# Optimization experiments

Hardware: AMD Instinct MI355X
Metric: run time of the kernel (lower is better)

Reference implementation:

```python
import jax, jax.numpy as jnp
import numpy as np

N = 100000
E = 1600000
IN_CH = 128
HID = 128
HEADS = 4
C = HID // HEADS  # 32 per-head channels
NUM_CLASSES = 40
NEG_SLOPE = 0.2


def _glorot(key, shape):
    fan_in, fan_out = shape[0], shape[-1]
    lim = jnp.sqrt(6.0 / (fan_in + fan_out))
    return jax.random.uniform(key, shape, jnp.float32, -lim, lim)


def setup_inputs() -> dict:
    key = jax.random.key(0)
    ks = jax.random.split(key, 12)
    x = jax.random.normal(ks[0], (N, IN_CH), jnp.float32)
    edge_index = jax.random.randint(ks[1], (2, E), 0, N, jnp.int64)
    edge_weight = jax.random.uniform(ks[2], (E,), jnp.float32)
    return {
        'x': x,
        'edge_index': edge_index,
        'edge_weight': edge_weight,
        'W_pre': _glorot(ks[3], (IN_CH, HID)),
        'Wl': _glorot(ks[4], (HID, HEADS * C)),
        'bl': jnp.zeros((HEADS * C,), jnp.float32),
        'Wr': _glorot(ks[5], (HID, HEADS * C)),
        'br': jnp.zeros((HEADS * C,), jnp.float32),
        'We': _glorot(ks[6], (1, HEADS * C)),
        'att': _glorot(ks[7], (HEADS, C)),
        'b_gat': jnp.zeros((HEADS * C,), jnp.float32),
        'W1': _glorot(ks[8], (HID, HID)),
        'b1': jnp.zeros((HID,), jnp.float32),
        'W2': _glorot(ks[9], (HID, NUM_CLASSES)),
        'b2': jnp.zeros((NUM_CLASSES,), jnp.float32),
    }


def reference(x, edge_index, edge_weight, W_pre, Wl, bl, Wr, br, We, att, b_gat, W1, b1, W2, b2):
    # pre projection (bias=False), norm = Identity
    h0 = x @ W_pre  # [N, HID]

    # --- GATv2Conv (PyG semantics, eval mode) ---
    # add self loops; self-loop edge_attr = mean of existing edge_attr (fill_value='mean')
    loop = jnp.arange(N, dtype=edge_index.dtype)
    src = jnp.concatenate([edge_index[0], loop])  # [E+N]
    dst = jnp.concatenate([edge_index[1], loop])
    ea = jnp.concatenate([edge_weight, jnp.full((N,), jnp.mean(edge_weight), edge_weight.dtype)])  # [E+N]

    x_l = (h0 @ Wl + bl).reshape(N, HEADS, C)  # source transform
    x_r = (h0 @ Wr + br).reshape(N, HEADS, C)  # target transform
    edge_emb = (ea[:, None] * We).reshape(-1, HEADS, C)  # lin_edge (bias=False)

    xj = x_l[src]  # [Etot, H, C] gather of source features
    e = jax.nn.leaky_relu(xj + x_r[dst] + edge_emb, NEG_SLOPE)
    alpha = jnp.einsum('ehc,hc->eh', e, att)  # [Etot, H]

    # segment softmax over destination neighborhoods
    amax = jax.ops.segment_max(alpha, dst, num_segments=N)
    amax = jnp.where(jnp.isfinite(amax), amax, 0.0)
    ex = jnp.exp(alpha - amax[dst])
    denom = jax.ops.segment_sum(ex, dst, num_segments=N)
    attn = ex / (denom[dst] + 1e-16)  # [Etot, H]

    out = jax.ops.segment_sum(attn[:, :, None] * xj, dst, num_segments=N)  # [N, H, C]
    out = out.reshape(N, HEADS * C) + b_gat

    h1 = jax.nn.elu(out)
    h = h0 + h1  # residual

    logits = jax.nn.relu(h @ W1 + b1) @ W2 + b2
    return h, logits
```

## Files before the change

### kernel.cpp

```cpp
#include <hip/hip_runtime.h>

typedef __attribute__((ext_vector_type(8))) short short8;
typedef __attribute__((ext_vector_type(16))) float f32x16;

#if __has_builtin(__builtin_amdgcn_exp2f)
#define EXP2(x) __builtin_amdgcn_exp2f(x)
#else
#define EXP2(x) exp2f(x)
#endif

static __device__ __forceinline__ unsigned short f2bf(float f){
  unsigned u = __float_as_uint(f);
  unsigned r = u + 0x7fffu + ((u >> 16) & 1u);
  return (unsigned short)(r >> 16);
}
static __device__ __forceinline__ float bf2f(unsigned short h){
  return __uint_as_float(((unsigned)h) << 16);
}

__global__ void wprep(const float* __restrict__ Wpre, const float* __restrict__ Wl,
                      const float* __restrict__ Wr, const float* __restrict__ W1,
                      const float* __restrict__ W2, const float* __restrict__ bl,
                      const float* __restrict__ br,
                      unsigned short* __restrict__ Phi, unsigned short* __restrict__ Plo,
                      unsigned short* __restrict__ Lhi, unsigned short* __restrict__ Llo,
                      unsigned short* __restrict__ W1hi, unsigned short* __restrict__ W1lo,
                      unsigned short* __restrict__ W2hi, unsigned short* __restrict__ W2lo,
                      float* __restrict__ bcat){
  int i = blockIdx.x*256 + threadIdx.x;
  float v; unsigned short* hp; unsigned short* lp; int oi;
  if (i < 16384){
    int c = i >> 7, k = i & 127;
    v = Wpre[(size_t)k*128 + c]; hp = Phi; lp = Plo; oi = i;
  } else if (i < 49152){
    int j = i - 16384; int c = j >> 7, k = j & 127;
    v = (c < 128) ? Wl[(size_t)k*128 + c] : Wr[(size_t)k*128 + (c-128)];
    hp = Lhi; lp = Llo; oi = j;
  } else if (i < 65536){
    int j = i - 49152; int c = j >> 7, k = j & 127;
    v = W1[(size_t)k*128 + c]; hp = W1hi; lp = W1lo; oi = j;
  } else if (i < 70656){
    int j = i - 65536; int c = j >> 7, k = j & 127;
    v = W2[(size_t)k*40 + c]; hp = W2hi; lp = W2lo; oi = j;
  } else if (i < 70912){
    int j = i - 70656;
    bcat[j] = (j < 128) ? bl[j] : br[j-128];
    return;
  } else return;
  unsigned short h = f2bf(v);
  hp[oi] = h;
  lp[oi] = f2bf(v - bf2f(h));
}

__global__ void count_mean(const int* __restrict__ ei, const float* __restrict__ ew,
                           int* __restrict__ deg, int* __restrict__ rk,
                           float* __restrict__ msum, int E){
  float s = 0.f;
  for (int e = blockIdx.x*256 + threadIdx.x; e < E; e += gridDim.x*256){
    rk[e] = atomicAdd(&deg[ei[E + e]], 1);
    s += ew[e];
  }
  for (int d = 32; d > 0; d >>= 1) s += __shfl_down(s, d, 64);
  __shared__ float ps[4];
  int lane = threadIdx.x & 63, w = threadIdx.x >> 6;
  if (lane == 0) ps[w] = s;
  __syncthreads();
  if (threadIdx.x == 0) atomicAdd(msum, (ps[0]+ps[1]+ps[2]+ps[3]) / (float)E);
}

__global__ __launch_bounds__(256) void scan1_kernel(const int* __restrict__ deg, int* __restrict__ rowptr,
                                                    int* __restrict__ bsum, int* __restrict__ dhist, int N){
  __shared__ int s[256];
  __shared__ int lhist[256];
  int i = blockIdx.x*256 + threadIdx.x;
  lhist[threadIdx.x] = 0;
  __syncthreads();
  int v = (i < N) ? deg[i] : 0;
  if (i < N) atomicAdd(&lhist[v < 255 ? v : 255], 1);
  s[threadIdx.x] = v;
  __syncthreads();
  for (int off = 1; off < 256; off <<= 1){
    int t = (threadIdx.x >= off) ? s[threadIdx.x - off] : 0;
    __syncthreads();
    s[threadIdx.x] += t;
    __syncthreads();
  }
  if (i < N) rowptr[i + 1] = s[threadIdx.x];
  if (threadIdx.x == 255) bsum[blockIdx.x] = s[255];
  int c = lhist[threadIdx.x];
  if (c > 0) atomicAdd(&dhist[threadIdx.x], c);
}

__global__ __launch_bounds__(512) void scan2_kernel(const int* __restrict__ bsum, int* __restrict__ boff, int nb,
                                                    const int* __restrict__ dhist, int* __restrict__ dhoff){
  __shared__ int s[512];
  __shared__ int s2[256];
  int v = (threadIdx.x < nb) ? bsum[threadIdx.x] : 0;
  s[threadIdx.x] = v;
  __syncthreads();
  for (int off = 1; off < 512; off <<= 1){
    int t = (threadIdx.x >= off) ? s[threadIdx.x - off] : 0;
    __syncthreads();
    s[threadIdx.x] += t;
    __syncthreads();
  }
  if (threadIdx.x < nb) boff[threadIdx.x] = s[threadIdx.x] - v;
  int v2 = 0;
  if (threadIdx.x < 256){ v2 = dhist[threadIdx.x]; s2[threadIdx.x] = v2; }
  __syncthreads();
  for (int off = 1; off < 256; off <<= 1){
    int t = 0;
    if (threadIdx.x < 256 && threadIdx.x >= off) t = s2[threadIdx.x - off];
    __syncthreads();
    if (threadIdx.x < 256) s2[threadIdx.x] += t;
    __syncthreads();
  }
  if (threadIdx.x < 256) dhoff[threadIdx.x] = s2[threadIdx.x] - v2;
}

__global__ __launch_bounds__(256) void scan3_kernel(int* __restrict__ rowptr, const int* __restrict__ boff,
                                                    const int* __restrict__ deg, int* __restrict__ dhoff,
                                                    int* __restrict__ perm, int N){
  __shared__ int lcnt[256];
  __shared__ int lbase[256];
  int i = blockIdx.x*256 + threadIdx.x;
  lcnt[threadIdx.x] = 0;
  __syncthreads();
  if (i == 0) rowptr[0] = 0;
  int d = 0, lr = 0;
  if (i < N){
    rowptr[i + 1] += boff[i >> 8];
    d = deg[i]; d = d < 255 ? d : 255;
    lr = atomicAdd(&lcnt[d], 1);
  }
  __syncthreads();
  int c = lcnt[threadIdx.x];
  if (c > 0) lbase[threadIdx.x] = atomicAdd(&dhoff[threadIdx.x], c);
  __syncthreads();
  if (i < N) perm[lbase[d] + lr] = i;
}

__global__ void fill_kernel(const int* __restrict__ ei, const float* __restrict__ ew,
                            const int* __restrict__ rowptr, const int* __restrict__ rk,
                            int2* __restrict__ erec, int E){
  int e = blockIdx.x*256 + threadIdx.x;
  if (e >= E) return;
  int dst = ei[E + e];
  erec[rowptr[dst] + rk[e]] = make_int2(ei[e], __float_as_int(ew[e]));
}

template<int NT>
static __device__ __forceinline__ void stageA(short* alds, const float* __restrict__ A,
                                              int row0, int N, int t){
  for (int g = t; g < 1024; g += NT){
    int r = g >> 4, k8 = g & 15;
    int grow = row0 + r;
    float4 p0, p1;
    if (grow < N){
      const float* ap = A + (size_t)grow*128 + k8*8;
      p0 = *(const float4*)ap;
      p1 = *(const float4*)(ap + 4);
    } else {
      p0 = make_float4(0.f,0.f,0.f,0.f); p1 = p0;
    }
    float vv[8] = {p0.x,p0.y,p0.z,p0.w,p1.x,p1.y,p1.z,p1.w};
    short8 hv, lv;
    #pragma unroll
    for (int j = 0; j < 8; ++j){
      unsigned short h = f2bf(vv[j]);
      hv[j] = (short)h;
      lv[j] = (short)f2bf(vv[j] - bf2f(h));
    }
    int slot = k8 ^ (r & 15);
    *(short8*)&alds[r*128 + slot*8] = hv;
    *(short8*)&alds[8192 + r*128 + slot*8] = lv;
  }
}

#define MFMA_KLOOP(ACC0, ACC1) \
  _Pragma("unroll") \
  for (int ks = 0; ks < 8; ++ks){ \
    int k8 = ks*2 + kg; \
    const short* a0 = &alds[r0*128 + (k8 ^ sx)*8]; \
    const short* a1 = &alds[(r0+32)*128 + (k8 ^ sx)*8]; \
    short8 a0h = *(const short8*)a0; \
    short8 a0l = *(const short8*)(a0 + 8192); \
    short8 a1h = *(const short8*)a1; \
    short8 a1l = *(const short8*)(a1 + 8192); \
    ACC0 = __builtin_amdgcn_mfma_f32_32x32x16_bf16(a0h, bh[ks],  ACC0, 0,0,0); \
    ACC1 = __builtin_amdgcn_mfma_f32_32x32x16_bf16(a1h, bh[ks],  ACC1, 0,0,0); \
    ACC0 = __builtin_amdgcn_mfma_f32_32x32x16_bf16(a0l, bh[ks],  ACC0, 0,0,0); \
    ACC1 = __builtin_amdgcn_mfma_f32_32x32x16_bf16(a1l, bh[ks],  ACC1, 0,0,0); \
    ACC0 = __builtin_amdgcn_mfma_f32_32x32x16_bf16(a0h, bl8[ks], ACC0, 0,0,0); \
    ACC1 = __builtin_amdgcn_mfma_f32_32x32x16_bf16(a1h, bl8[ks], ACC1, 0,0,0); \
  }

__global__ __launch_bounds__(512) void pre_kernel(
    const float* __restrict__ A,
    const unsigned short* __restrict__ Phi, const unsigned short* __restrict__ Plo,
    const unsigned short* __restrict__ Lhi, const unsigned short* __restrict__ Llo,
    const float* __restrict__ bcat,
    float* __restrict__ hout, unsigned short* __restrict__ xlr, int N)
{
  __shared__ short alds[2*64*128];
  const int t = threadIdx.x;
  const int row0 = blockIdx.x * 64;
  stageA<512>(alds, A, row0, N, t);
  __syncthreads();

  const int lane = t & 63, w = t >> 6;
  const int cl = lane & 31, kg = lane >> 5;
  const int sx = cl & 15;

  {
    const int rt = w & 1, ct = w >> 1;
    const int colp = ct*32 + cl;
    short8 bh[8], bl8[8];
    #pragma unroll
    for (int ks = 0; ks < 8; ++ks){
      size_t off = (size_t)colp*128 + ks*16 + kg*8;
      bh[ks]  = *(const short8*)(Phi + off);
      bl8[ks] = *(const short8*)(Plo + off);
    }
    f32x16 acc;
    #pragma unroll
    for (int i = 0; i < 16; ++i) acc[i] = 0.f;
    const int r0 = rt*32 + cl;
    #pragma unroll
    for (int ks = 0; ks < 8; ++ks){
      int k8 = ks*2 + kg;
      const short* a = &alds[r0*128 + (k8 ^ sx)*8];
      short8 ah = *(const short8*)a;
      short8 al = *(const short8*)(a + 8192);
      acc = __builtin_amdgcn_mfma_f32_32x32x16_bf16(ah, bh[ks],  acc, 0,0,0);
      acc = __builtin_amdgcn_mfma_f32_32x32x16_bf16(al, bh[ks],  acc, 0,0,0);
      acc = __builtin_amdgcn_mfma_f32_32x32x16_bf16(ah, bl8[ks], acc, 0,0,0);
    }
    __syncthreads();
    #pragma unroll
    for (int reg = 0; reg < 16; ++reg){
      int row = rt*32 + (reg & 3) + 8*(reg >> 2) + 4*kg;
      float v = acc[reg];
      int grow = row0 + row;
      if (grow < N) hout[(size_t)grow*128 + colp] = v;
      unsigned short h = f2bf(v);
      unsigned short l = f2bf(v - bf2f(h));
      int idx = row*128 + (((colp >> 3) ^ (row & 15)) << 3) + (colp & 7);
      alds[idx] = (short)h;
      alds[8192 + idx] = (short)l;
    }
  }
  __syncthreads();

  {
    const int col = w*32 + cl;
    short8 bh[8], bl8[8];
    #pragma unroll
    for (int ks = 0; ks < 8; ++ks){
      size_t off = (size_t)col*128 + ks*16 + kg*8;
      bh[ks]  = *(const short8*)(Lhi + off);
      bl8[ks] = *(const short8*)(Llo + off);
    }
    f32x16 acc0, acc1;
    #pragma unroll
    for (int i = 0; i < 16; ++i){ acc0[i] = 0.f; acc1[i] = 0.f; }
    const int r0 = cl;
    MFMA_KLOOP(acc0, acc1)
    float bv = bcat[col];
    #pragma unroll
    for (int rt2 = 0; rt2 < 2; ++rt2){
      const f32x16& ac = rt2 ? acc1 : acc0;
      #pragma unroll
      for (int reg = 0; reg < 16; ++reg){
        int row = rt2*32 + (reg & 3) + 8*(reg >> 2) + 4*kg;
        int grow = row0 + row;
        if (grow < N) xlr[(size_t)grow*256 + col] = f2bf(ac[reg] + bv);
      }
    }
  }
}

__global__ __launch_bounds__(256) void mlp_kernel(
    const float* __restrict__ A,
    const unsigned short* __restrict__ B1hi, const unsigned short* __restrict__ B1lo,
    const float* __restrict__ b1,
    const unsigned short* __restrict__ B2hi, const unsigned short* __restrict__ B2lo,
    const float* __restrict__ b2,
    float* __restrict__ logits, int N)
{
  __shared__ short alds[2*64*128];
  const int t = threadIdx.x;
  const int row0 = blockIdx.x * 64;
  stageA<256>(alds, A, row0, N, t);
  __syncthreads();

  const int lane = t & 63, w = t >> 6;
  const int cl = lane & 31, kg = lane >> 5;
  const int r0 = cl;
  const int sx = r0 & 15;

  {
    const int col = w*32 + cl;
    short8 bh[8], bl8[8];
    #pragma unroll
    for (int ks = 0; ks < 8; ++ks){
      size_t off = (size_t)col*128 + ks*16 + kg*8;
      bh[ks]  = *(const short8*)(B1hi + off);
      bl8[ks] = *(const short8*)(B1lo + off);
    }
    f32x16 acc0, acc1;
    #pragma unroll
    for (int i = 0; i < 16; ++i){ acc0[i] = 0.f; acc1[i] = 0.f; }
    MFMA_KLOOP(acc0, acc1)

    float bv = b1[col];
    __syncthreads();
    #pragma unroll
    for (int rt = 0; rt < 2; ++rt){
      const f32x16& ac = rt ? acc1 : acc0;
      #pragma unroll
      for (int reg = 0; reg < 16; ++reg){
        int row = rt*32 + (reg & 3) + 8*(reg >> 2) + 4*kg;
        float v = fmaxf(ac[reg] + bv, 0.f);
        unsigned short h = f2bf(v);
        unsigned short l = f2bf(v - bf2f(h));
        int idx = row*128 + (((col >> 3) ^ (row & 15)) << 3) + (col & 7);
        alds[idx] = (short)h;
        alds[8192 + idx] = (short)l;
      }
    }
    __syncthreads();
  }

  if (w < 2){
    const int col = w*32 + cl;
    const bool cok = col < 40;
    short8 bh[8], bl8[8];
    #pragma unroll
    for (int ks = 0; ks < 8; ++ks){
      if (cok){
        size_t off = (size_t)col*128 + ks*16 + kg*8;
        bh[ks]  = *(const short8*)(B2hi + off);
        bl8[ks] = *(const short8*)(B2lo + off);
      } else {
        #pragma unroll
        for (int j = 0; j < 8; ++j){ bh[ks][j] = 0; bl8[ks][j] = 0; }
      }
    }
    f32x16 acc0, acc1;
    #pragma unroll
    for (int i = 0; i < 16; ++i){ acc0[i] = 0.f; acc1[i] = 0.f; }
    MFMA_KLOOP(acc0, acc1)

    if (cok){
      float bv = b2[col];
      #pragma unroll
      for (int rt = 0; rt < 2; ++rt){
        const f32x16& ac = rt ? acc1 : acc0;
        #pragma unroll
        for (int reg = 0; reg < 16; ++reg){
          int row = rt*32 + (reg & 3) + 8*(reg >> 2) + 4*kg;
          int grow = row0 + row;
          if (grow < N) logits[(size_t)grow*40 + col] = ac[reg] + bv;
        }
      }
    }
  }
}

__global__ __launch_bounds__(256) void gather_kernel(
    const int* __restrict__ rowptr, const int2* __restrict__ erec,
    const unsigned short* __restrict__ xlr,
    const int* __restrict__ perm,
    const float* __restrict__ We, const float* __restrict__ att,
    const float* __restrict__ msum, const float* __restrict__ bgat,
    float* __restrict__ hbuf, int N)
{
  const int wid  = threadIdx.x >> 6;
  const int lane = threadIdx.x & 63;
  const int g    = lane >> 4;
  const int l    = lane & 15;
  const int ch0  = l * 8;
  const int slot = (blockIdx.x*4 + wid)*4 + g;
  const bool nok = slot < N;
  const int n    = nok ? perm[slot] : 0;

  float xrv[8], wev[8], at6[8], at4[8];
  {
    short8 q = *(const short8*)&xlr[(size_t)n*256 + 128 + ch0];
    float4 w0 = *(const float4*)&We[ch0];
    float4 w1 = *(const float4*)&We[ch0+4];
    float4 a0 = *(const float4*)&att[ch0];
    float4 a1 = *(const float4*)&att[ch0+4];
    const float L2E = 1.4426950408889634f;
    float wv[8] = {w0.x,w0.y,w0.z,w0.w,w1.x,w1.y,w1.z,w1.w};
    float av[8] = {a0.x,a0.y,a0.z,a0.w,a1.x,a1.y,a1.z,a1.w};
    #pragma unroll
    for (int j = 0; j < 8; ++j){
      xrv[j] = bf2f((unsigned short)q[j]);
      wev[j] = wv[j];
      at6[j] = av[j]*0.6f*L2E;
      at4[j] = av[j]*0.4f*L2E;
    }
  }

  float num[8];
  #pragma unroll
  for (int j = 0; j < 8; ++j) num[j] = 0.f;
  float den = 0.f;

  const float wm = msum[0];
  int beg = 0, end = 0;
  if (nok){ beg = rowptr[n]; end = rowptr[n + 1]; }
  const int cnt = nok ? (end - beg + 1) : 0;

  int itMax = cnt;
  itMax = max(itMax, __shfl_xor(itMax, 16, 64));
  itMax = max(itMax, __shfl_xor(itMax, 32, 64));

  const int2 selfrec = make_int2(n, __float_as_int(wm));

  int pos = beg;
  int2 rec0 = (pos     < end) ? erec[pos]     : selfrec;
  int2 rec1 = (pos + 1 < end) ? erec[pos + 1] : selfrec;
  int2 rec2 = (pos + 2 < end) ? erec[pos + 2] : selfrec;
  short8 pv0 = *(const short8*)&xlr[(size_t)rec0.x*256 + ch0];
  short8 pv1 = *(const short8*)&xlr[(size_t)rec1.x*256 + ch0];
  short8 pv2 = *(const short8*)&xlr[(size_t)rec2.x*256 + ch0];

  for (int it = 0; it < itMax; it += 2){
    int2 rec3 = (pos + 3 < end) ? erec[pos + 3] : selfrec;
    int2 rec4 = (pos + 4 < end) ? erec[pos + 4] : selfrec;
    short8 pv3 = *(const short8*)&xlr[(size_t)rec3.x*256 + ch0];
    short8 pv4 = *(const short8*)&xlr[(size_t)rec4.x*256 + ch0];

    {
      const bool act = it < cnt;
      const float wj = __int_as_float(rec0.y);
      float xlv[8];
      #pragma unroll
      for (int q = 0; q < 8; ++q) xlv[q] = bf2f((unsigned short)pv0[q]);
      float p = 0.f;
      #pragma unroll
      for (int q = 0; q < 8; ++q){
        float z = fmaf(wj, wev[q], xlv[q] + xrv[q]);
        p = fmaf(at6[q], z, p);
        p = fmaf(at4[q], fabsf(z), p);
      }
      p += __shfl_xor(p, 1, 64);
      p += __shfl_xor(p, 2, 64);
      float ex = act ? EXP2(p) : 0.f;
      den += ex;
      #pragma unroll
      for (int q = 0; q < 8; ++q) num[q] = fmaf(ex, xlv[q], num[q]);
    }
    {
      const bool act = (it + 1) < cnt;
      const float wj = __int_as_float(rec1.y);
      float xlv[8];
      #pragma unroll
      for (int q = 0; q < 8; ++q) xlv[q] = bf2f((unsigned short)pv1[q]);
      float p = 0.f;
      #pragma unroll
      for (int q = 0; q < 8; ++q){
        float z = fmaf(wj, wev[q], xlv[q] + xrv[q]);
        p = fmaf(at6[q], z, p);
        p = fmaf(at4[q], fabsf(z), p);
      }
      p += __shfl_xor(p, 1, 64);
      p += __shfl_xor(p, 2, 64);
      float ex = act ? EXP2(p) : 0.f;
      den += ex;
      #pragma unroll
      for (int q = 0; q < 8; ++q) num[q] = fmaf(ex, xlv[q], num[q]);
    }

    rec0 = rec2; rec1 = rec3; rec2 = rec4;
    pv0 = pv2;  pv1 = pv3;  pv2 = pv4;
    pos += 2;
  }

  if (nok){
    float inv = 1.f / (den + 1e-16f);
    float o[8];
    #pragma unroll
    for (int j = 0; j < 8; ++j){
      float v = num[j]*inv + bgat[ch0+j];
      o[j] = v > 0.f ? v : expm1f(v);
    }
    float4 h0a = *(const float4*)&hbuf[(size_t)n*128 + ch0];
    float4 h0b = *(const float4*)&hbuf[(size_t)n*128 + ch0 + 4];
    h0a.x += o[0]; h0a.y += o[1]; h0a.z += o[2]; h0a.w += o[3];
    h0b.x += o[4]; h0b.y += o[5]; h0b.z += o[6]; h0b.w += o[7];
    *(float4*)&hbuf[(size_t)n*128 + ch0]     = h0a;
    *(float4*)&hbuf[(size_t)n*128 + ch0 + 4] = h0b;
  }
}

extern "C" void kernel_launch(void* const* d_in, const int* in_sizes, int n_in,
                              void* d_out, int out_size, void* d_ws, size_t ws_size,
                              hipStream_t stream)
{
  const float* x    = (const float*)d_in[0];
  const int*   ei   = (const int*)  d_in[1];
  const float* ew   = (const float*)d_in[2];
  const float* Wpre = (const float*)d_in[3];
  const float* Wl   = (const float*)d_in[4];
  const float* bl   = (const float*)d_in[5];
  const float* Wr   = (const float*)d_in[6];
  const float* br   = (const float*)d_in[7];
  const float* We   = (const float*)d_in[8];
  const float* att  = (const float*)d_in[9];
  const float* bgat = (const float*)d_in[10];
  const float* W1   = (const float*)d_in[11];
  const float* b1   = (const float*)d_in[12];
  const float* W2   = (const float*)d_in[13];
  const float* b2   = (const float*)d_in[14];

  const int N = in_sizes[0] / 128;
  const int E = in_sizes[2];
  const int nb = (N + 255) / 256;

  float* hout   = (float*)d_out;
  float* logits = hout + (size_t)N*128;

  unsigned short* xlr = (unsigned short*)d_ws;
  int2*  erec   = (int2*)(xlr + (size_t)N*256);
  int*   rk     = (int*)(erec + E);
  int*   rowptr = rk + E;
  int*   cursor = rowptr + N + 1;
  float* msum   = (float*)(cursor + N);
  int*   dhist  = (int*)(msum + 1);
  int*   bsum   = dhist + 256;
  int*   boff   = bsum + nb;
  int*   dhoff  = boff + nb;
  int*   perm   = dhoff + 256;
  float* bcat   = (float*)(perm + N);
  unsigned short* wsp = (unsigned short*)(((uintptr_t)(bcat + 256) + 15) & ~(uintptr_t)15);
  unsigned short* Phi  = wsp;
  unsigned short* Plo  = Phi + 16384;
  unsigned short* Lhi  = Plo + 16384;
  unsigned short* Llo  = Lhi + 32768;
  unsigned short* W1hi = Llo + 32768;
  unsigned short* W1lo = W1hi + 16384;
  unsigned short* W2hi = W1lo + 16384;
  unsigned short* W2lo = W2hi + 5120;

  hipMemsetAsync(cursor, 0, (size_t)(N + 1 + 256) * sizeof(int), stream);

  wprep<<<278, 256, 0, stream>>>(Wpre, Wl, Wr, W1, W2, bl, br,
                                 Phi, Plo, Lhi, Llo, W1hi, W1lo, W2hi, W2lo, bcat);
  count_mean<<<1024, 256, 0, stream>>>(ei, ew, cursor, rk, msum, E);
  scan1_kernel<<<nb, 256, 0, stream>>>(cursor, rowptr, bsum, dhist, N);
  scan2_kernel<<<1, 512, 0, stream>>>(bsum, boff, nb, dhist, dhoff);
  scan3_kernel<<<nb, 256, 0, stream>>>(rowptr, boff, cursor, dhoff, perm, N);
  fill_kernel<<<(E + 255)/256, 256, 0, stream>>>(ei, ew, rowptr, rk, erec, E);

  const int gg = (N + 63) / 64;
  pre_kernel<<<gg, 512, 0, stream>>>(x, Phi, Plo, Lhi, Llo, bcat, hout, xlr, N);

  gather_kernel<<<(N + 15)/16, 256, 0, stream>>>(rowptr, erec, xlr, perm, We, att, msum, bgat, hout, N);

  mlp_kernel<<<gg, 256, 0, stream>>>(hout, W1hi, W1lo, b1, W2hi, W2lo, b2, logits, N);
}
```

Before: 318.9 us.

## Fold W_pre into Wl/Wr and run both projections in one MFMA pass

```diff
diff --git a/kernel.cpp b/kernel.cpp
--- a/kernel.cpp
+++ b/kernel.cpp
@@ -18,38 +18,52 @@
   return __uint_as_float(((unsigned)h) << 16);
 }
 
-__global__ void wprep(const float* __restrict__ Wpre, const float* __restrict__ Wl,
-                      const float* __restrict__ Wr, const float* __restrict__ W1,
+__global__ void wprep(const float* __restrict__ Wpre, const float* __restrict__ W1,
                       const float* __restrict__ W2, const float* __restrict__ bl,
                       const float* __restrict__ br,
-                      unsigned short* __restrict__ Phi, unsigned short* __restrict__ Plo,
-                      unsigned short* __restrict__ Lhi, unsigned short* __restrict__ Llo,
-                      unsigned short* __restrict__ W1hi, unsigned short* __restrict__ W1lo,
-                      unsigned short* __restrict__ W2hi, unsigned short* __restrict__ W2lo,
+                      unsigned short* __restrict__ PhiF, unsigned short* __restrict__ PloF,
+                      unsigned short* __restrict__ W1hiF, unsigned short* __restrict__ W1loF,
+                      unsigned short* __restrict__ W2hiF, unsigned short* __restrict__ W2loF,
                       float* __restrict__ bcat){
   int i = blockIdx.x*256 + threadIdx.x;
-  float v; unsigned short* hp; unsigned short* lp; int oi;
+  float v; unsigned short* hp; unsigned short* lp; size_t idx;
   if (i < 16384){
-    int c = i >> 7, k = i & 127;
-    v = Wpre[(size_t)k*128 + c]; hp = Phi; lp = Plo; oi = i;
-  } else if (i < 49152){
-    int j = i - 16384; int c = j >> 7, k = j & 127;
-    v = (c < 128) ? Wl[(size_t)k*128 + c] : Wr[(size_t)k*128 + (c-128)];
-    hp = Lhi; lp = Llo; oi = j;
-  } else if (i < 65536){
-    int j = i - 49152; int c = j >> 7, k = j & 127;
-    v = W1[(size_t)k*128 + c]; hp = W1hi; lp = W1lo; oi = j;
-  } else if (i < 70656){
-    int j = i - 65536; int c = j >> 7, k = j & 127;
-    v = W2[(size_t)k*40 + c]; hp = W2hi; lp = W2lo; oi = j;
-  } else if (i < 70912){
-    int j = i - 70656;
+    int k = i >> 7, c = i & 127;
+    v = Wpre[i]; hp = PhiF; lp = PloF;
+    idx = ((size_t)(k>>3)*128 + c)*8 + (k&7);
+  } else if (i < 32768){
+    int j = i - 16384; int k = j >> 7, c = j & 127;
+    v = W1[j]; hp = W1hiF; lp = W1loF;
+    idx = ((size_t)(k>>3)*128 + c)*8 + (k&7);
+  } else if (i < 37888){
+    int j = i - 32768; int k = j / 40, c = j % 40;
+    v = W2[j]; hp = W2hiF; lp = W2loF;
+    idx = ((size_t)(k>>3)*40 + c)*8 + (k&7);
+  } else if (i < 38144){
+    int j = i - 37888;
     bcat[j] = (j < 128) ? bl[j] : br[j-128];
     return;
   } else return;
   unsigned short h = f2bf(v);
-  hp[oi] = h;
-  lp[oi] = f2bf(v - bf2f(h));
+  hp[idx] = h;
+  lp[idx] = f2bf(v - bf2f(h));
+}
+
+__global__ __launch_bounds__(256) void wcomb_kernel(
+    const float* __restrict__ Wpre, const float* __restrict__ Wl,
+    const float* __restrict__ Wr,
+    unsigned short* __restrict__ ChiF, unsigned short* __restrict__ CloF){
+  int tid = blockIdx.x*256 + threadIdx.x;
+  int r = tid >> 8;
+  int c = tid & 255;
+  const float* B = (c < 128) ? (Wl + c) : (Wr + (c - 128));
+  float s = 0.f;
+  for (int k = 0; k < 128; ++k)
+    s = fmaf(Wpre[r*128 + k], B[(size_t)k*128], s);
+  unsigned short h = f2bf(s);
+  size_t idx = ((size_t)(r>>3)*256 + c)*8 + (r&7);
+  ChiF[idx] = h;
+  CloF[idx] = f2bf(s - bf2f(h));
 }
 
 __global__ void count_mean(const int* __restrict__ ei, const float* __restrict__ ew,
@@ -195,77 +209,55 @@
     ACC1 = __builtin_amdgcn_mfma_f32_32x32x16_bf16(a1h, bl8[ks], ACC1, 0,0,0); \
   }
 
-__global__ __launch_bounds__(512) void pre_kernel(
+__global__ __launch_bounds__(768) void pre_kernel(
     const float* __restrict__ A,
-    const unsigned short* __restrict__ Phi, const unsigned short* __restrict__ Plo,
-    const unsigned short* __restrict__ Lhi, const unsigned short* __restrict__ Llo,
+    const unsigned short* __restrict__ PhiF, const unsigned short* __restrict__ PloF,
+    const unsigned short* __restrict__ ChiF, const unsigned short* __restrict__ CloF,
     const float* __restrict__ bcat,
     float* __restrict__ hout, unsigned short* __restrict__ xlr, int N)
 {
   __shared__ short alds[2*64*128];
   const int t = threadIdx.x;
   const int row0 = blockIdx.x * 64;
-  stageA<512>(alds, A, row0, N, t);
-  __syncthreads();
-
   const int lane = t & 63, w = t >> 6;
   const int cl = lane & 31, kg = lane >> 5;
   const int sx = cl & 15;
-
-  {
-    const int rt = w & 1, ct = w >> 1;
-    const int colp = ct*32 + cl;
-    short8 bh[8], bl8[8];
-    #pragma unroll
-    for (int ks = 0; ks < 8; ++ks){
-      size_t off = (size_t)colp*128 + ks*16 + kg*8;
-      bh[ks]  = *(const short8*)(Phi + off);
-      bl8[ks] = *(const short8*)(Plo + off);
-    }
-    f32x16 acc;
-    #pragma unroll
-    for (int i = 0; i < 16; ++i) acc[i] = 0.f;
-    const int r0 = rt*32 + cl;
-    #pragma unroll
-    for (int ks = 0; ks < 8; ++ks){
-      int k8 = ks*2 + kg;
-      const short* a = &alds[r0*128 + (k8 ^ sx)*8];
-      short8 ah = *(const short8*)a;
-      short8 al = *(const short8*)(a + 8192);
-      acc = __builtin_amdgcn_mfma_f32_32x32x16_bf16(ah, bh[ks],  acc, 0,0,0);
-      acc = __builtin_amdgcn_mfma_f32_32x32x16_bf16(al, bh[ks],  acc, 0,0,0);
-      acc = __builtin_amdgcn_mfma_f32_32x32x16_bf16(ah, bl8[ks], acc, 0,0,0);
-    }
-    __syncthreads();
-    #pragma unroll
-    for (int reg = 0; reg < 16; ++reg){
-      int row = rt*32 + (reg & 3) + 8*(reg >> 2) + 4*kg;
-      float v = acc[reg];
-      int grow = row0 + row;
-      if (grow < N) hout[(size_t)grow*128 + colp] = v;
-      unsigned short h = f2bf(v);
-      unsigned short l = f2bf(v - bf2f(h));
-      int idx = row*128 + (((colp >> 3) ^ (row & 15)) << 3) + (colp & 7);
-      alds[idx] = (short)h;
-      alds[8192 + idx] = (short)l;
-    }
-  }
-  __syncthreads();
-
-  {
-    const int col = w*32 + cl;
-    short8 bh[8], bl8[8];
-    #pragma unroll
-    for (int ks = 0; ks < 8; ++ks){
-      size_t off = (size_t)col*128 + ks*16 + kg*8;
-      bh[ks]  = *(const short8*)(Lhi + off);
-      bl8[ks] = *(const short8*)(Llo + off);
-    }
-    f32x16 acc0, acc1;
-    #pragma unroll
-    for (int i = 0; i < 16; ++i){ acc0[i] = 0.f; acc1[i] = 0.f; }
-    const int r0 = cl;
-    MFMA_KLOOP(acc0, acc1)
+  const int S = w * 32;
+  const bool isP = S < 128;
+  const int col = isP ? (S + cl) : (S - 128 + cl);
+  const int NC  = isP ? 128 : 256;
+  const unsigned short* Bhi = isP ? PhiF : ChiF;
+  const unsigned short* Blo = isP ? PloF : CloF;
+
+  short8 bh[8], bl8[8];
+  #pragma unroll
+  for (int ks = 0; ks < 8; ++ks){
+    size_t off = ((size_t)(ks*2 + kg)*NC + col)*8;
+    bh[ks]  = *(const short8*)(Bhi + off);
+    bl8[ks] = *(const short8*)(Blo + off);
+  }
+
+  stageA<768>(alds, A, row0, N, t);
+  __syncthreads();
+
+  f32x16 acc0, acc1;
+  #pragma unroll
+  for (int i = 0; i < 16; ++i){ acc0[i] = 0.f; acc1[i] = 0.f; }
+  const int r0 = cl;
+  MFMA_KLOOP(acc0, acc1)
+
+  if (isP){
+    #pragma unroll
+    for (int rt2 = 0; rt2 < 2; ++rt2){
+      const f32x16& ac = rt2 ? acc1 : acc0;
+      #pragma unroll
+      for (int reg = 0; reg < 16; ++reg){
+        int row = rt2*32 + (reg & 3) + 8*(reg >> 2) + 4*kg;
+        int grow = row0 + row;
+        if (grow < N) hout[(size_t)grow*128 + col] = ac[reg];
+      }
+    }
+  } else {
     float bv = bcat[col];
     #pragma unroll
     for (int rt2 = 0; rt2 < 2; ++rt2){
@@ -304,7 +296,7 @@
     short8 bh[8], bl8[8];
     #pragma unroll
     for (int ks = 0; ks < 8; ++ks){
-      size_t off = (size_t)col*128 + ks*16 + kg*8;
+      size_t off = ((size_t)(ks*2 + kg)*128 + col)*8;
       bh[ks]  = *(const short8*)(B1hi + off);
       bl8[ks] = *(const short8*)(B1lo + off);
     }
@@ -339,7 +331,7 @@
     #pragma unroll
     for (int ks = 0; ks < 8; ++ks){
       if (cok){
-        size_t off = (size_t)col*128 + ks*16 + kg*8;
+        size_t off = ((size_t)(ks*2 + kg)*40 + col)*8;
         bh[ks]  = *(const short8*)(B2hi + off);
         bl8[ks] = *(const short8*)(B2lo + off);
       } else {
@@ -537,19 +529,20 @@
   int*   perm   = dhoff + 256;
   float* bcat   = (float*)(perm + N);
   unsigned short* wsp = (unsigned short*)(((uintptr_t)(bcat + 256) + 15) & ~(uintptr_t)15);
-  unsigned short* Phi  = wsp;
-  unsigned short* Plo  = Phi + 16384;
-  unsigned short* Lhi  = Plo + 16384;
-  unsigned short* Llo  = Lhi + 32768;
-  unsigned short* W1hi = Llo + 32768;
-  unsigned short* W1lo = W1hi + 16384;
-  unsigned short* W2hi = W1lo + 16384;
-  unsigned short* W2lo = W2hi + 5120;
+  unsigned short* PhiF  = wsp;
+  unsigned short* PloF  = PhiF + 16384;
+  unsigned short* ChiF  = PloF + 16384;
+  unsigned short* CloF  = ChiF + 32768;
+  unsigned short* W1hiF = CloF + 32768;
+  unsigned short* W1loF = W1hiF + 16384;
+  unsigned short* W2hiF = W1loF + 16384;
+  unsigned short* W2loF = W2hiF + 5120;
 
   hipMemsetAsync(cursor, 0, (size_t)(N + 1 + 256) * sizeof(int), stream);
 
-  wprep<<<278, 256, 0, stream>>>(Wpre, Wl, Wr, W1, W2, bl, br,
-                                 Phi, Plo, Lhi, Llo, W1hi, W1lo, W2hi, W2lo, bcat);
+  wprep<<<150, 256, 0, stream>>>(Wpre, W1, W2, bl, br,
+                                 PhiF, PloF, W1hiF, W1loF, W2hiF, W2loF, bcat);
+  wcomb_kernel<<<128, 256, 0, stream>>>(Wpre, Wl, Wr, ChiF, CloF);
   count_mean<<<1024, 256, 0, stream>>>(ei, ew, cursor, rk, msum, E);
   scan1_kernel<<<nb, 256, 0, stream>>>(cursor, rowptr, bsum, dhist, N);
   scan2_kernel<<<1, 512, 0, stream>>>(bsum, boff, nb, dhist, dhoff);
@@ -557,9 +550,9 @@
   fill_kernel<<<(E + 255)/256, 256, 0, stream>>>(ei, ew, rowptr, rk, erec, E);
 
   const int gg = (N + 63) / 64;
-  pre_kernel<<<gg, 512, 0, stream>>>(x, Phi, Plo, Lhi, Llo, bcat, hout, xlr, N);
+  pre_kernel<<<gg, 768, 0, stream>>>(x, PhiF, PloF, ChiF, CloF, bcat, hout, xlr, N);
 
   gather_kernel<<<(N + 15)/16, 256, 0, stream>>>(rowptr, erec, xlr, perm, We, att, msum, bgat, hout, N);
 
-  mlp_kernel<<<gg, 256, 0, stream>>>(hout, W1hi, W1lo, b1, W2hi, W2lo, b2, logits, N);
-}
+  mlp_kernel<<<gg, 256, 0, stream>>>(hout, W1hiF, W1loF, b1, W2hiF, W2loF, b2, logits, N);
+}
```

Result: no change. 319.4 us (+0.1%).
